# Kernel optimization log

Measured on AMD Instinct MI355X. Metric: run time of the kernel, lower is better.

The kernel has to match this reference:

```python
import jax, jax.numpy as jnp
import numpy as np

B, S, N, M, D = 1, 8, 768, 768, 64
K, RATIO, IT, THR = 8, 0.6, 16, 0.75
R_N, R_M = int(RATIO * N), int(RATIO * M)


def _solver(sx, sy, sm):
    # mask-weighted cross-correlation model: (Bi, D, D)
    w = sm.astype(sx.dtype)
    num = jnp.einsum('bnd,bnm,bme->bde', sx, w, sy)
    den = jnp.sum(w, axis=(-2, -1))[:, None, None] + 1e-6
    return num / den


def _evaluator(models, x, y, mask):
    # squared L2 residual ||x @ model - y||^2, NaN where mask is False -> (Bi, N, M)
    xt = jnp.einsum('bnd,bde->bne', x, models)
    sq = (jnp.sum(xt * xt, -1)[:, :, None] + jnp.sum(y * y, -1)[:, None, :]
          - 2.0 * jnp.einsum('bne,bme->bnm', xt, y))
    return jnp.where(mask, sq, jnp.nan)


def _ransac(x, y, mask, perm1, perm2):
    Bi, n, d = x.shape
    m = y.shape[1]
    p1 = perm1.reshape(-1)  # (IT*R_N,) values in [0, R_N)
    p2 = perm2.reshape(-1)
    s_x = x[:, p1].reshape(Bi * IT, R_N, d)
    s_y = y[:, p2].reshape(Bi * IT, R_M, d)
    s_m = mask[:, p1].reshape(Bi, IT, R_N, m)
    s_m = jnp.take_along_axis(s_m, perm2[None, :, None, :], axis=-1)
    s_m = s_m.reshape(Bi * IT, R_N, R_M)
    models = _solver(s_x, s_y, s_m)  # (Bi*IT, D, D)
    xr = jnp.broadcast_to(x[:, None], (Bi, IT, n, d)).reshape(Bi * IT, n, d)
    yr = jnp.broadcast_to(y[:, None], (Bi, IT, m, d)).reshape(Bi * IT, m, d)
    mr = jnp.broadcast_to(mask[:, None], (Bi, IT, n, m)).reshape(Bi * IT, n, m)
    errors = _evaluator(models, xr, yr, mr).reshape(Bi, IT, n, m)
    models = models.reshape(Bi, IT, D, D)
    avg = jnp.nanmean(errors, axis=(-1, -2))  # (Bi, IT)
    best = jnp.argmin(avg, axis=-1)
    best_model = jnp.take_along_axis(models, best[:, None, None, None], axis=1)[:, 0]
    best_errors = jnp.take_along_axis(errors, best[:, None, None, None], axis=1)[:, 0]
    thrs = jnp.nanquantile(best_errors, THR, axis=-1, keepdims=True)
    inliers = best_errors < thrs
    return best_model, inliers, best_errors


def _forward(qk, kks, qmask, kmask, perm1, perm2):
    mask = qmask & kmask  # (B*S, N, M)
    x = jnp.broadcast_to(qk[:, None], (B, S, N, D)).reshape(B * S, N, D)
    y = kks.reshape(B * S, M, D)
    bm, inl, be = _ransac(x, y, mask, perm1, perm2)
    bm = bm.reshape(B, S, D, D)
    inl = inl.reshape(B, S, N, M)
    be = be.reshape(B, S, N, M)
    avg = jnp.nanmean(be, axis=(-2, -1))  # (B, S)
    topk_err, topk_idx = jax.lax.top_k(avg, K)  # torch.topk default: largest
    tm = jnp.take_along_axis(bm, topk_idx[:, :, None, None], axis=1)
    ti = jnp.take_along_axis(inl, topk_idx[:, :, None, None], axis=1)
    return ti, tm, topk_err


def setup_inputs() -> dict:
    key = jax.random.key(0)
    k1, k2, k3, k4, k5, k6 = jax.random.split(key, 6)
    qk = jax.random.normal(k1, (B, N, D), jnp.float32)
    kks = jax.random.normal(k2, (B, S, M, D), jnp.float32)
    qmask = jax.random.randint(k3, (B * S, N, M), 0, 2) > 0
    kmask = jax.random.randint(k4, (B * S, N, M), 0, 2) > 0
    # _batch_randperm: permutations of [0, r_n)
    perm1 = jnp.argsort(jax.random.uniform(k5, (IT, R_N)), axis=-1).astype(jnp.int32)
    perm2 = jnp.argsort(jax.random.uniform(k6, (IT, R_M)), axis=-1).astype(jnp.int32)
    return {"qk": qk, "kks": kks, "qmask": qmask, "kmask": kmask,
            "perm1": perm1, "perm2": perm2}


def reference(qk, kks, qmask, kmask, perm1, perm2):
    return _forward(qk, kks, qmask, kmask, perm1, perm2)
```

## Files before the change

kernel.cpp:

```cpp
#include <hip/hip_runtime.h>
#include <math.h>

#define NN 768
#define MM 768
#define DD 64
#define BI 8
#define RN 460
#define KTOP 8

static constexpr size_t OFF_TI = 0;
static constexpr size_t OFF_TM = (size_t)KTOP * NN * MM;
static constexpr size_t OFF_TE = OFF_TM + (size_t)KTOP * DD * DD;

static constexpr size_t TP_OFF    = 0;
static constexpr size_t NUMP_OFF  = TP_OFF + (size_t)8 * BI * RN * DD;
static constexpr size_t MODEL_OFF = NUMP_OFF + (size_t)32 * BI * DD * DD;
static constexpr size_t XT_OFF    = MODEL_OFF + (size_t)BI * DD * DD;
static constexpr size_t ERR_OFF   = XT_OFF + (size_t)BI * NN * DD;
static constexpr size_t FEND      = ERR_OFF + (size_t)BI * NN * MM;
static constexpr size_t ESUM_B = FEND * 4;
static constexpr size_t ECNT_B = ESUM_B + 1152 * 4;
static constexpr size_t DENP_B = ECNT_B + 1152 * 4;
static constexpr size_t PM_B   = DENP_B + 512 * 4 + 32;

__device__ __forceinline__ int ldm(const void* p, int flag, size_t idx) {
  if (flag) return ((const int*)p)[idx] != 0;
  return ((const unsigned char*)p)[idx] != 0;
}

__device__ __forceinline__ unsigned f2key(float f) {
  unsigned u = __float_as_uint(f);
  return (u & 0x80000000u) ? ~u : (u | 0x80000000u);
}
__device__ __forceinline__ float key2f(unsigned k) {
  unsigned u = (k & 0x80000000u) ? (k ^ 0x80000000u) : ~k;
  return __uint_as_float(u);
}

__global__ __launch_bounds__(256) void k_tgemm(
    const float* __restrict__ kks, const void* __restrict__ qm, const void* __restrict__ km,
    float* __restrict__ tpart, int* __restrict__ denp, unsigned long long* __restrict__ pmw) {
  __shared__ float ys[64 * 68];
  __shared__ int cntsh[4];
  __shared__ int flg[4];
  const int tid = threadIdx.x, lane = tid & 63, g = tid >> 6;
  const int ntile = blockIdx.x, c = blockIdx.y, b = blockIdx.z;

  {
    unsigned w0 = ((const unsigned*)qm)[tid];
    unsigned long long any = __ballot((w0 & 0xFFFFFF00u) != 0);
    if (lane == 0) flg[g] = (any != 0) ? 1 : 0;
  }
  __syncthreads();
  const int flag = (flg[0] | flg[1] | flg[2] | flg[3]) ? 0 : 1;

  const int m0 = c * 64;
  const float* yb = kks + (size_t)b * MM * DD;
  for (int q = tid; q < 1024; q += 256) {
    int r = q >> 4, col = (q & 15) * 4;
    *(float4*)&ys[r * 68 + col] = *(const float4*)&yb[(size_t)(m0 + r) * DD + col];
  }
  const int n0 = ntile * 64 + g * 16;
  unsigned wlo[16], whi[16];
  int cnt = 0;
#pragma unroll
  for (int i = 0; i < 16; i++) {
    int n = n0 + i;
    size_t idx = ((size_t)b * NN + n) * MM + m0 + lane;
    int cm = ldm(qm, flag, idx) & ldm(km, flag, idx);
    unsigned long long w = __ballot(cm);
    if (lane == 0) pmw[((size_t)b * NN + n) * 12 + c] = w;
    if (c == 7) w &= 0xFFFULL;
    wlo[i] = (unsigned)w; whi[i] = (unsigned)(w >> 32);
    if (n < RN) cnt += __builtin_popcountll(w);
  }
  __syncthreads();
  float acc[16];
#pragma unroll
  for (int i = 0; i < 16; i++) acc[i] = 0.f;
#pragma unroll 4
  for (int m = 0; m < 32; m++) {
    int yi = __float_as_int(ys[m * 68 + lane]);
#pragma unroll
    for (int i = 0; i < 16; i++) {
      int sel = ((int)(wlo[i] << (31 - m))) >> 31;
      acc[i] += __int_as_float(yi & sel);
    }
  }
#pragma unroll 4
  for (int m = 0; m < 32; m++) {
    int yi = __float_as_int(ys[(m + 32) * 68 + lane]);
#pragma unroll
    for (int i = 0; i < 16; i++) {
      int sel = ((int)(whi[i] << (31 - m))) >> 31;
      acc[i] += __int_as_float(yi & sel);
    }
  }
#pragma unroll
  for (int i = 0; i < 16; i++) {
    int n = n0 + i;
    if (n < RN)
      tpart[(((size_t)c * BI + b) * RN + n) * DD + lane] = acc[i];
  }
  if (lane == 0) cntsh[g] = cnt;
  __syncthreads();
  if (tid == 0) denp[(b * 8 + c) * 8 + ntile] = cntsh[0] + cntsh[1] + cntsh[2] + cntsh[3];

  {
    int ebase = (c * 8 + ntile) * 80 + g * 20;
    for (int k = 0; k < 20; k++) {
      int eidx = ebase + k;
      int n, w;
      if (eidx < 3072) { n = 512 + eidx / 12; w = eidx % 12; }
      else             { int r = eidx - 3072; n = r >> 2; w = 8 + (r & 3); }
      size_t idx = ((size_t)b * NN + n) * MM + w * 64 + lane;
      int cm = ldm(qm, flag, idx) & ldm(km, flag, idx);
      unsigned long long bl = __ballot(cm);
      if (lane == 0) pmw[((size_t)b * NN + n) * 12 + w] = bl;
    }
  }
}

__global__ __launch_bounds__(256) void k_num(
    const float* __restrict__ qk, const float* __restrict__ tpart, float* __restrict__ numpart) {
  __shared__ float xs[16 * 64];
  __shared__ float ts[16 * 64];
  const int tid = threadIdx.x, lane = tid & 63, g = tid >> 6;
  const int chunk = blockIdx.x, b = blockIdx.y;
  for (int l = tid; l < 1024; l += 256) {
    int r = l >> 6, col = l & 63;
    int n = chunk * 16 + r;
    float xv = 0.f, tv = 0.f;
    if (n < RN) {
      xv = qk[(size_t)n * DD + col];
#pragma unroll
      for (int cc = 0; cc < 8; cc++)
        tv += tpart[(((size_t)cc * BI + b) * RN + n) * DD + col];
    }
    xs[l] = xv; ts[l] = tv;
  }
  __syncthreads();
  float acc[16];
#pragma unroll
  for (int i = 0; i < 16; i++) acc[i] = 0.f;
#pragma unroll 4
  for (int r = 0; r < 16; r++) {
    float tv = ts[r * 64 + lane];
#pragma unroll
    for (int i = 0; i < 16; i++) acc[i] += xs[r * 64 + g + i * 4] * tv;
  }
#pragma unroll
  for (int i = 0; i < 16; i++)
    numpart[((size_t)chunk * BI + b) * (DD * DD) + (size_t)(g + i * 4) * DD + lane] = acc[i];
}

__global__ __launch_bounds__(256) void k_model(
    const float* __restrict__ numpart, const int* __restrict__ denp, float* __restrict__ model) {
  __shared__ float invp;
  const int tid = threadIdx.x;
  const int b = blockIdx.x >> 3, part = blockIdx.x & 7;
  if (tid < 64) {
    int v = denp[b * 64 + tid];
#pragma unroll
    for (int o = 32; o > 0; o >>= 1) v += __shfl_xor(v, o);
    if (tid == 0) invp = 1.f / ((float)v + 1e-6f);
  }
  __syncthreads();
  float inv = invp;
  for (int l = part * 512 + tid; l < part * 512 + 512; l += 256) {
    float s = 0.f;
#pragma unroll
    for (int cc = 0; cc < 32; cc++) s += numpart[((size_t)cc * BI + b) * (DD * DD) + l];
    model[(size_t)b * (DD * DD) + l] = s * inv;
  }
}

__global__ __launch_bounds__(256) void k_xt(
    const float* __restrict__ qk, const float* __restrict__ model, float* __restrict__ xt) {
  __shared__ float ml[DD * DD];
  const int tid = threadIdx.x, lane = tid & 63, g = tid >> 6;
  const int seg = blockIdx.x, b = blockIdx.y;
  const float4* msrc = (const float4*)(model + (size_t)b * DD * DD);
  for (int q = tid; q < 1024; q += 256) ((float4*)ml)[q] = msrc[q];
  __syncthreads();
#pragma unroll
  for (int rr = 0; rr < 6; rr++) {
    int n = seg * 24 + g * 6 + rr;
    float acc = 0.f;
#pragma unroll 8
    for (int d = 0; d < DD; d++) acc += qk[(size_t)n * DD + d] * ml[d * DD + lane];
    xt[((size_t)b * NN + n) * DD + lane] = acc;
  }
}

__global__ __launch_bounds__(256) void k_err(
    const float* __restrict__ xt, const float* __restrict__ kks,
    const unsigned long long* __restrict__ pmw,
    float* __restrict__ err, float* __restrict__ esum, int* __restrict__ ecnt) {
  __shared__ float As[64 * 68];
  __shared__ float Bs[64 * 68];
  __shared__ float xx[64], yy[64];
  __shared__ float rsum[256];
  __shared__ int rcnt[256];
  const int b = blockIdx.z, wj = blockIdx.x;
  const int i0 = blockIdx.y * 64, j0 = wj * 64;
  const int tid = threadIdx.x, tx = tid & 15, ty = tid >> 4;
  const float* xb = xt + ((size_t)b * NN + i0) * DD;
  const float* yb = kks + ((size_t)b * MM + j0) * DD;
  for (int q = tid; q < 1024; q += 256) {
    int r = q >> 4, c = q & 15;
    *(float4*)&As[r * 68 + c * 4] = ((const float4*)(xb + (size_t)r * DD))[c];
    *(float4*)&Bs[r * 68 + c * 4] = ((const float4*)(yb + (size_t)r * DD))[c];
  }
  __syncthreads();
  if (tid < 64) {
    float s = 0.f;
#pragma unroll 8
    for (int k2 = 0; k2 < 64; k2++) { float v = As[tid * 68 + k2]; s += v * v; }
    xx[tid] = s;
  } else if (tid < 128) {
    int r = tid - 64;
    float s = 0.f;
#pragma unroll 8
    for (int k2 = 0; k2 < 64; k2++) { float v = Bs[r * 68 + k2]; s += v * v; }
    yy[r] = s;
  }
  __syncthreads();
  float acc[4][4];
#pragma unroll
  for (int ii = 0; ii < 4; ii++)
#pragma unroll
    for (int jj = 0; jj < 4; jj++) acc[ii][jj] = 0.f;
  for (int k2 = 0; k2 < 64; k2 += 4) {
    float4 av[4], bv[4];
#pragma unroll
    for (int ii = 0; ii < 4; ii++) av[ii] = *(const float4*)&As[(ty + 16 * ii) * 68 + k2];
#pragma unroll
    for (int jj = 0; jj < 4; jj++) bv[jj] = *(const float4*)&Bs[(tx + 16 * jj) * 68 + k2];
#pragma unroll
    for (int ii = 0; ii < 4; ii++)
#pragma unroll
      for (int jj = 0; jj < 4; jj++)
        acc[ii][jj] += av[ii].x * bv[jj].x + av[ii].y * bv[jj].y +
                       av[ii].z * bv[jj].z + av[ii].w * bv[jj].w;
  }
  float psum = 0.f;
  int pcnt = 0;
#pragma unroll
  for (int ii = 0; ii < 4; ii++) {
    int i = i0 + ty + 16 * ii;
    unsigned long long word = pmw[((size_t)b * NN + i) * 12 + wj];
    size_t rowb = ((size_t)b * NN + i) * MM;
#pragma unroll
    for (int jj = 0; jj < 4; jj++) {
      int j = j0 + tx + 16 * jj;
      int cm = (int)((word >> (tx + 16 * jj)) & 1ULL);
      float v = xx[ty + 16 * ii] + yy[tx + 16 * jj] - 2.f * acc[ii][jj];
      if (cm) { err[rowb + j] = v; psum += v; pcnt++; }
    }
  }
  rsum[tid] = psum;
  rcnt[tid] = pcnt;
  __syncthreads();
  for (int s = 128; s > 0; s >>= 1) {
    if (tid < s) { rsum[tid] += rsum[tid + s]; rcnt[tid] += rcnt[tid + s]; }
    __syncthreads();
  }
  if (tid == 0) {
    int t = b * 144 + blockIdx.y * 12 + wj;
    esum[t] = rsum[0];
    ecnt[t] = rcnt[0];
  }
}

__global__ __launch_bounds__(256) void k_quant(
    const float* __restrict__ err, const unsigned long long* __restrict__ pmw,
    const float* __restrict__ esum, const int* __restrict__ ecnt,
    const float* __restrict__ model, float* __restrict__ out) {
  __shared__ float avg_sh[BI];
  __shared__ int ords_sh[BI];
  const int bid = blockIdx.x, tid = threadIdx.x, lane = tid & 63, g = tid >> 6;
  const float INF = __builtin_inff();
  for (int h = 0; h < 2; h++) {
    int b = g * 2 + h, base = b * 144;
    float s = esum[base + lane] + esum[base + 64 + lane] + ((lane < 16) ? esum[base + 128 + lane] : 0.f);
    int ct = ecnt[base + lane] + ecnt[base + 64 + lane] + ((lane < 16) ? ecnt[base + 128 + lane] : 0);
#pragma unroll
    for (int o = 32; o > 0; o >>= 1) { s += __shfl_xor(s, o); ct += __shfl_xor(ct, o); }
    if (lane == 0) avg_sh[b] = s / (float)ct;
  }
  __syncthreads();
  if (tid == 0) {
    unsigned used = 0;
#pragma unroll
    for (int k = 0; k < KTOP; k++) {
      int best = 0;
      float bv = -INF;
#pragma unroll
      for (int b = 0; b < BI; b++)
        if (!((used >> b) & 1u) && avg_sh[b] > bv) { bv = avg_sh[b]; best = b; }
      used |= 1u << best;
      ords_sh[k] = best;
    }
  }
  __syncthreads();
  if (bid == 0) {
    if (tid < KTOP) out[OFF_TE + tid] = avg_sh[ords_sh[tid]];
    for (int l = tid; l < KTOP * DD * DD; l += 256) {
      int k = l >> 12;
      out[OFF_TM + l] = model[(size_t)ords_sh[k] * (DD * DD) + (l & (DD * DD - 1))];
    }
  }
  const int kk = bid >> 6, seg = bid & 63;
  const int b = ords_sh[kk];
  for (int rr = 0; rr < 3; rr++) {
    int n = seg * 12 + g * 3 + rr;
    const float* row = err + ((size_t)b * NN + n) * MM;
    size_t prow = ((size_t)b * NN + n) * 12;
    unsigned long long wd[3];
#pragma unroll
    for (int w = 0; w < 3; w++) wd[w] = pmw[prow + w * 4 + (lane >> 4)];
    int cp = (lane < 12) ? __builtin_popcountll(pmw[prow + lane]) : 0;
#pragma unroll
    for (int o = 32; o > 0; o >>= 1) cp += __shfl_xor(cp, o);
    const int cnt = cp;
    float v[12];
#pragma unroll
    for (int w = 0; w < 3; w++) {
      float4 f4 = ((const float4*)row)[w * 64 + lane];
      v[w * 4 + 0] = f4.x; v[w * 4 + 1] = f4.y; v[w * 4 + 2] = f4.z; v[w * 4 + 3] = f4.w;
    }
    unsigned key[12];
    unsigned mnk = 0xFFFFFFFFu, mxk = 0u;
#pragma unroll
    for (int r = 0; r < 12; r++) {
      int bit = (int)((wd[r >> 2] >> (((lane & 15) << 2) + (r & 3))) & 1ULL);
      unsigned kf = f2key(v[r]);
      key[r] = bit ? kf : 0xFFFFFFFFu;
      mnk = min(mnk, key[r]);
      mxk = max(mxk, bit ? kf : 0u);
    }
#pragma unroll
    for (int o = 32; o > 0; o >>= 1) {
      mnk = min(mnk, (unsigned)__shfl_xor((int)mnk, o));
      mxk = max(mxk, (unsigned)__shfl_xor((int)mxk, o));
    }
    float thr;
    if (cnt == 0) {
      thr = -INF;
    } else {
      float pos = 0.75f * (float)(cnt - 1);
      int k0 = (int)pos;
      float f = pos - (float)k0;
      int target = k0 + 1;
      unsigned lo = mnk, hi = mxk;
      while (lo < hi) {
        unsigned mid = lo + ((hi - lo) >> 1);
        int c = 0;
#pragma unroll
        for (int r = 0; r < 12; r++) c += __builtin_popcountll(__ballot(key[r] <= mid));
        if (c >= target) hi = mid; else lo = mid + 1;
      }
      unsigned ka = lo;
      float a = key2f(ka);
      float b2;
      if (k0 + 1 >= cnt) {
        b2 = a;
      } else {
        int c1 = 0;
#pragma unroll
        for (int r = 0; r < 12; r++) c1 += __builtin_popcountll(__ballot(key[r] <= ka));
        if (c1 >= k0 + 2) {
          b2 = a;
        } else {
          unsigned mn = 0xFFFFFFFFu;
#pragma unroll
          for (int r = 0; r < 12; r++) mn = min(mn, (key[r] > ka) ? key[r] : 0xFFFFFFFFu);
#pragma unroll
          for (int o = 32; o > 0; o >>= 1) mn = min(mn, (unsigned)__shfl_xor((int)mn, o));
          b2 = key2f(mn);
        }
      }
      thr = a + f * (b2 - a);
    }
    float* orow = out + OFF_TI + ((size_t)kk * NN + n) * MM;
#pragma unroll
    for (int w = 0; w < 3; w++) {
      unsigned long long ww = wd[w];
      int sh = (lane & 15) << 2;
      float4 o;
      o.x = (((ww >> (sh + 0)) & 1ULL) && v[w * 4 + 0] < thr) ? 1.f : 0.f;
      o.y = (((ww >> (sh + 1)) & 1ULL) && v[w * 4 + 1] < thr) ? 1.f : 0.f;
      o.z = (((ww >> (sh + 2)) & 1ULL) && v[w * 4 + 2] < thr) ? 1.f : 0.f;
      o.w = (((ww >> (sh + 3)) & 1ULL) && v[w * 4 + 3] < thr) ? 1.f : 0.f;
      ((float4*)orow)[w * 64 + lane] = o;
    }
  }
}

extern "C" void kernel_launch(void* const* d_in, const int* in_sizes, int n_in,
                              void* d_out, int out_size, void* d_ws, size_t ws_size,
                              hipStream_t stream) {
  (void)in_sizes; (void)n_in; (void)out_size; (void)ws_size;
  const float* qk  = (const float*)d_in[0];
  const float* kks = (const float*)d_in[1];
  const void*  qm  = d_in[2];
  const void*  km  = d_in[3];
  float* out = (float*)d_out;
  float* wsf = (float*)d_ws;
  char*  wsb = (char*)d_ws;
  float* tpart   = wsf + TP_OFF;
  float* numpart = wsf + NUMP_OFF;
  float* model   = wsf + MODEL_OFF;
  float* xtb     = wsf + XT_OFF;
  float* errb    = wsf + ERR_OFF;
  float* esum = (float*)(wsb + ESUM_B);
  int*   ecnt = (int*)(wsb + ECNT_B);
  int*   denp = (int*)(wsb + DENP_B);
  unsigned long long* pmw = (unsigned long long*)(wsb + PM_B);

  k_tgemm<<<dim3(8, 8, BI), 256, 0, stream>>>(kks, qm, km, tpart, denp, pmw);
  k_num<<<dim3(32, BI), 256, 0, stream>>>(qk, tpart, numpart);
  k_model<<<64, 256, 0, stream>>>(numpart, denp, model);
  k_xt<<<dim3(32, BI), 256, 0, stream>>>(qk, model, xtb);
  k_err<<<dim3(12, 12, BI), 256, 0, stream>>>(xtb, kks, pmw, errb, esum, ecnt);
  k_quant<<<512, 256, 0, stream>>>(errb, pmw, esum, ecnt, model, out);
}
```

Baseline: 195.7 us.

## Split mask bit-packing into dedicated vectorized kernel feeding tgemm

```diff
diff --git a/kernel.cpp b/kernel.cpp
--- a/kernel.cpp
+++ b/kernel.cpp
@@ -23,11 +23,6 @@
 static constexpr size_t DENP_B = ECNT_B + 1152 * 4;
 static constexpr size_t PM_B   = DENP_B + 512 * 4 + 32;
 
-__device__ __forceinline__ int ldm(const void* p, int flag, size_t idx) {
-  if (flag) return ((const int*)p)[idx] != 0;
-  return ((const unsigned char*)p)[idx] != 0;
-}
-
 __device__ __forceinline__ unsigned f2key(float f) {
   unsigned u = __float_as_uint(f);
   return (u & 0x80000000u) ? ~u : (u | 0x80000000u);
@@ -37,15 +32,12 @@
   return __uint_as_float(u);
 }
 
-__global__ __launch_bounds__(256) void k_tgemm(
-    const float* __restrict__ kks, const void* __restrict__ qm, const void* __restrict__ km,
-    float* __restrict__ tpart, int* __restrict__ denp, unsigned long long* __restrict__ pmw) {
-  __shared__ float ys[64 * 68];
-  __shared__ int cntsh[4];
+__global__ __launch_bounds__(256) void k_pack(
+    const void* __restrict__ qm, const void* __restrict__ km,
+    unsigned long long* __restrict__ pmw) {
+  __shared__ __align__(16) unsigned char nib[768];
   __shared__ int flg[4];
   const int tid = threadIdx.x, lane = tid & 63, g = tid >> 6;
-  const int ntile = blockIdx.x, c = blockIdx.y, b = blockIdx.z;
-
   {
     unsigned w0 = ((const unsigned*)qm)[tid];
     unsigned long long any = __ballot((w0 & 0xFFFFFF00u) != 0);
@@ -53,7 +45,55 @@
   }
   __syncthreads();
   const int flag = (flg[0] | flg[1] | flg[2] | flg[3]) ? 0 : 1;
-
+  const int rg = blockIdx.x, b = blockIdx.y;
+  const size_t E0 = ((size_t)b * NN + (size_t)rg * 4) * MM;
+  unsigned nb[3];
+#pragma unroll
+  for (int k = 0; k < 3; k++) {
+    int gi = tid + 256 * k;
+    size_t e = E0 + 4 * (size_t)gi;
+    unsigned nibble;
+    if (flag) {
+      uint4 qa = *(const uint4*)((const int*)qm + e);
+      uint4 ka = *(const uint4*)((const int*)km + e);
+      nibble = ((qa.x && ka.x) ? 1u : 0u) | ((qa.y && ka.y) ? 2u : 0u) |
+               ((qa.z && ka.z) ? 4u : 0u) | ((qa.w && ka.w) ? 8u : 0u);
+    } else {
+      unsigned qa = *(const unsigned*)((const unsigned char*)qm + e);
+      unsigned ka = *(const unsigned*)((const unsigned char*)km + e);
+      nibble = (((qa & 0xFFu) && (ka & 0xFFu)) ? 1u : 0u) |
+               (((qa & 0xFF00u) && (ka & 0xFF00u)) ? 2u : 0u) |
+               (((qa & 0xFF0000u) && (ka & 0xFF0000u)) ? 4u : 0u) |
+               (((qa & 0xFF000000u) && (ka & 0xFF000000u)) ? 8u : 0u);
+    }
+    nb[k] = nibble;
+  }
+#pragma unroll
+  for (int k = 0; k < 3; k++) nib[tid + 256 * k] = (unsigned char)nb[k];
+  __syncthreads();
+  if (tid < 48) {
+    uint4 q4 = *(const uint4*)&nib[tid * 16];
+    unsigned long long w = 0;
+    unsigned dw[4] = {q4.x, q4.y, q4.z, q4.w};
+#pragma unroll
+    for (int q = 0; q < 4; q++) {
+      w |= (unsigned long long)(dw[q] & 0xFu) << (16 * q + 0);
+      w |= (unsigned long long)((dw[q] >> 8) & 0xFu) << (16 * q + 4);
+      w |= (unsigned long long)((dw[q] >> 16) & 0xFu) << (16 * q + 8);
+      w |= (unsigned long long)((dw[q] >> 24) & 0xFu) << (16 * q + 12);
+    }
+    int n = rg * 4 + tid / 12, ww = tid % 12;
+    pmw[((size_t)b * NN + n) * 12 + ww] = w;
+  }
+}
+
+__global__ __launch_bounds__(256) void k_tgemm(
+    const float* __restrict__ kks, const unsigned long long* __restrict__ pmw,
+    float* __restrict__ tpart, int* __restrict__ denp) {
+  __shared__ float ys[64 * 68];
+  __shared__ int cntsh[4];
+  const int tid = threadIdx.x, lane = tid & 63, g = tid >> 6;
+  const int ntile = blockIdx.x, c = blockIdx.y, b = blockIdx.z;
   const int m0 = c * 64;
   const float* yb = kks + (size_t)b * MM * DD;
   for (int q = tid; q < 1024; q += 256) {
@@ -66,10 +106,7 @@
 #pragma unroll
   for (int i = 0; i < 16; i++) {
     int n = n0 + i;
-    size_t idx = ((size_t)b * NN + n) * MM + m0 + lane;
-    int cm = ldm(qm, flag, idx) & ldm(km, flag, idx);
-    unsigned long long w = __ballot(cm);
-    if (lane == 0) pmw[((size_t)b * NN + n) * 12 + c] = w;
+    unsigned long long w = pmw[((size_t)b * NN + n) * 12 + c];
     if (c == 7) w &= 0xFFFULL;
     wlo[i] = (unsigned)w; whi[i] = (unsigned)(w >> 32);
     if (n < RN) cnt += __builtin_popcountll(w);
@@ -105,20 +142,6 @@
   if (lane == 0) cntsh[g] = cnt;
   __syncthreads();
   if (tid == 0) denp[(b * 8 + c) * 8 + ntile] = cntsh[0] + cntsh[1] + cntsh[2] + cntsh[3];
-
-  {
-    int ebase = (c * 8 + ntile) * 80 + g * 20;
-    for (int k = 0; k < 20; k++) {
-      int eidx = ebase + k;
-      int n, w;
-      if (eidx < 3072) { n = 512 + eidx / 12; w = eidx % 12; }
-      else             { int r = eidx - 3072; n = r >> 2; w = 8 + (r & 3); }
-      size_t idx = ((size_t)b * NN + n) * MM + w * 64 + lane;
-      int cm = ldm(qm, flag, idx) & ldm(km, flag, idx);
-      unsigned long long bl = __ballot(cm);
-      if (lane == 0) pmw[((size_t)b * NN + n) * 12 + w] = bl;
-    }
-  }
 }
 
 __global__ __launch_bounds__(256) void k_num(
@@ -419,7 +442,8 @@
   int*   denp = (int*)(wsb + DENP_B);
   unsigned long long* pmw = (unsigned long long*)(wsb + PM_B);
 
-  k_tgemm<<<dim3(8, 8, BI), 256, 0, stream>>>(kks, qm, km, tpart, denp, pmw);
+  k_pack<<<dim3(192, BI), 256, 0, stream>>>(qm, km, pmw);
+  k_tgemm<<<dim3(8, 8, BI), 256, 0, stream>>>(kks, pmw, tpart, denp);
   k_num<<<dim3(32, BI), 256, 0, stream>>>(qk, tpart, numpart);
   k_model<<<64, 256, 0, stream>>>(numpart, denp, model);
   k_xt<<<dim3(32, BI), 256, 0, stream>>>(qk, model, xtb);
```

After: 178.4 us. 1.1x faster.
